# Performance work log

Measured on AMD Instinct MI355X. Metric: run time of the kernel, lower is better.

Reference implementation:

```python
import jax, jax.numpy as jnp
import numpy as np

B, N, C, H = 2, 8192, 256, 8  # Dh == C (attention_head_size = embedding_channels)
EPS = 1e-5  # InstanceNorm2d default eps


def setup_inputs() -> dict:
    key = jax.random.key(0)
    k1, k2, k3, k4, k5 = jax.random.split(key, 5)
    s = 1.0 / np.sqrt(C)
    return {
        "emb": jax.random.normal(k1, (B, N, C), dtype=jnp.float32),
        "Wq": jax.random.normal(k2, (C, C * H), dtype=jnp.float32) * s,
        "Wk": jax.random.normal(k3, (C, C * H), dtype=jnp.float32) * s,
        "Wv": jax.random.normal(k4, (C, C * H), dtype=jnp.float32) * s,
        "Wo": jax.random.normal(k5, (C * H, C), dtype=jnp.float32) * s,
    }


def reference(emb, Wq, Wk, Wv, Wo):
    b, n, c = emb.shape
    h = Wq.shape[1] // c  # num_heads; head_dim Dh == c

    def heads(x):  # [B,N,H*Dh] -> [B,H,N,Dh]
        return x.reshape(b, n, h, c).transpose(0, 2, 1, 3)

    qh = heads(emb @ Wq)  # [B,H,N,Dh]
    kh = heads(emb @ Wk)
    vh = heads(emb @ Wv)

    # channel attention: contract over sequence dim N -> [B,H,Dh,Dh]
    attn = jnp.einsum("bhnd,bhne->bhde", qh, kh)

    # InstanceNorm2d over the Dh x Dh map per (b,h), affine=False, biased var
    mu = attn.mean(axis=(2, 3), keepdims=True)
    var = attn.var(axis=(2, 3), keepdims=True)
    attn = (attn - mu) * jax.lax.rsqrt(var + EPS)

    attn = jax.nn.softmax(attn, axis=3)

    # attn @ v^T -> [B,H,Dh,N]
    ctx = jnp.einsum("bhde,bhne->bhdn", attn, vh)

    # permute(0,3,2,1) -> [B,N,Dh,H], flatten (Dh,H) -> KV_size
    ctx = ctx.transpose(0, 3, 2, 1).reshape(b, n, c * h)
    return ctx @ Wo  # [B,N,C]
```

## Files before the change

### kernel.cpp

```cpp
#include <hip/hip_runtime.h>
#include <hip/hip_bf16.h>

#define NB 2
#define NN 8192
#define NC 256
#define NH 8
#define NCH 2048

static constexpr float EPS = 1e-5f;


typedef __attribute__((ext_vector_type(8))) short bf16x8;
typedef __attribute__((ext_vector_type(4))) float f32x4;

#define MFMA16(a, b, c) __builtin_amdgcn_mfma_f32_16x16x32_bf16(a, b, c, 0, 0, 0)

static constexpr int ETH  = 0;
static constexpr int ETL  = 4194304;
static constexpr int WQTH = 8388608;
static constexpr int WQTL = 8912896;
static constexpr int WKTH = 9437184;
static constexpr int WKTL = 9961472;
static constexpr int WVH  = 10485760;
static constexpr int WVL  = 11010048;
static constexpr int WORH = 11534336;
static constexpr int WORL = 12058624;
static constexpr int GHH  = 12582912;
static constexpr int GHL  = 12713984;
static constexpr int T1H  = 12845056;
static constexpr int T1L  = 13893632;
static constexpr int SMH  = 14942208;
static constexpr int SML  = 15990784;
static constexpr int PTH  = 17039360;
static constexpr int PTL  = 17170432;


__device__ __forceinline__ ushort bf16rn(float x) {
    uint u = __float_as_uint(x);
    return (ushort)((u + 0x7fffu + ((u >> 16) & 1u)) >> 16);
}
__device__ __forceinline__ float bf2f(ushort h) { return __uint_as_float(((uint)h) << 16); }

__device__ __forceinline__ void stage64(ushort* __restrict__ lds, const ushort* __restrict__ src,
                                        int row0, int k0, int ld) {
    int t = threadIdx.x;
    int g = t & 7, r = t >> 3;
#pragma unroll
    for (int i = 0; i < 2; ++i, r += 32) {
        uint4 v = *(const uint4*)(src + (row0 + r) * ld + k0 + g * 8);
        *(uint4*)((char*)lds + r * 128 + ((g ^ (r & 7)) << 4)) = v;
    }
}

__device__ __forceinline__ void stage64_f32(ushort* __restrict__ ldsh, ushort* __restrict__ ldsl,
                                            const float* __restrict__ src, int row0, int k0, int ld) {
    int t = threadIdx.x;
    int g = t & 15, r = t >> 4;
#pragma unroll
    for (int i = 0; i < 4; ++i, r += 16) {
        float4 v = *(const float4*)(src + (row0 + r) * ld + k0 + g * 4);
        ushort h0 = bf16rn(v.x), h1 = bf16rn(v.y), h2 = bf16rn(v.z), h3 = bf16rn(v.w);
        ushort e0 = bf16rn(v.x - bf2f(h0)), e1 = bf16rn(v.y - bf2f(h1));
        ushort e2 = bf16rn(v.z - bf2f(h2)), e3 = bf16rn(v.w - bf2f(h3));
        int byte = r * 128 + ((((g >> 1) ^ (r & 7)) << 4) | ((g & 1) << 3));
        ushort4 hv = {h0, h1, h2, h3}, lv = {e0, e1, e2, e3};
        *(ushort4*)((char*)ldsh + byte) = hv;
        *(ushort4*)((char*)ldsl + byte) = lv;
    }
}

__device__ __forceinline__ bf16x8 frag64(const ushort* __restrict__ lds, int rbase, int ks) {
    int l = threadIdx.x & 63;
    int r = rbase + (l & 15);
    int slot = (ks * 4 + (l >> 4)) ^ (r & 7);
    return *(const bf16x8*)((const char*)lds + r * 128 + slot * 16);
}

__device__ __forceinline__ void mfma_tile(const ushort* Ah, const ushort* Al,
                                          const ushort* Bh, const ushort* Bl,
                                          int wm, int wn, f32x4 acc[2][2]) {
#pragma unroll
    for (int ks = 0; ks < 2; ++ks) {
        bf16x8 ah[2], al[2], bh[2], bl[2];
        ah[0] = frag64(Ah, wm, ks);      ah[1] = frag64(Ah, wm + 16, ks);
        al[0] = frag64(Al, wm, ks);      al[1] = frag64(Al, wm + 16, ks);
        bh[0] = frag64(Bh, wn, ks);      bh[1] = frag64(Bh, wn + 16, ks);
        bl[0] = frag64(Bl, wn, ks);      bl[1] = frag64(Bl, wn + 16, ks);
#pragma unroll
        for (int mi = 0; mi < 2; ++mi)
#pragma unroll
            for (int ni = 0; ni < 2; ++ni) {
                acc[mi][ni] = MFMA16(ah[mi], bh[ni], acc[mi][ni]);
                acc[mi][ni] = MFMA16(ah[mi], bl[ni], acc[mi][ni]);
                acc[mi][ni] = MFMA16(al[mi], bh[ni], acc[mi][ni]);
            }
    }
}

__device__ __forceinline__ void gemm_core(const ushort* Ahi, const ushort* Alo, int arow0, int lda, int k0a,
                                          const ushort* Bhi, const ushort* Blo, int brow0, int ldb, int k0b,
                                          int nkt, ushort* lds, f32x4 acc[2][2]) {
    ushort* Ah = lds; ushort* Al = lds + 4096; ushort* Bh = lds + 8192; ushort* Bl = lds + 12288;
    int w = threadIdx.x >> 6;
    int wm = (w >> 1) * 32, wn = (w & 1) * 32;
    for (int t = 0; t < nkt; ++t) {
        stage64(Ah, Ahi, arow0, k0a + t * 64, lda);
        stage64(Al, Alo, arow0, k0a + t * 64, lda);
        stage64(Bh, Bhi, brow0, k0b + t * 64, ldb);
        stage64(Bl, Blo, brow0, k0b + t * 64, ldb);
        __syncthreads();
        mfma_tile(Ah, Al, Bh, Bl, wm, wn, acc);
        __syncthreads();
    }
}

__device__ __forceinline__ void ep_hilo(ushort* Dh, ushort* Dl, int ld, int row0, int col0, f32x4 acc[2][2]) {
    int l = threadIdx.x & 63, w = threadIdx.x >> 6;
    int wm = (w >> 1) * 32, wn = (w & 1) * 32;
#pragma unroll
    for (int mi = 0; mi < 2; ++mi)
#pragma unroll
        for (int ni = 0; ni < 2; ++ni)
#pragma unroll
            for (int r = 0; r < 4; ++r) {
                float x = acc[mi][ni][r];
                int idx = (row0 + wm + mi * 16 + (l >> 4) * 4 + r) * ld + col0 + wn + ni * 16 + (l & 15);
                ushort h = bf16rn(x);
                Dh[idx] = h;
                Dl[idx] = bf16rn(x - bf2f(h));
            }
}

__device__ __forceinline__ void ep_f32(float* D, int ld, int row0, int col0, f32x4 acc[2][2]) {
    int l = threadIdx.x & 63, w = threadIdx.x >> 6;
    int wm = (w >> 1) * 32, wn = (w & 1) * 32;
#pragma unroll
    for (int mi = 0; mi < 2; ++mi)
#pragma unroll
        for (int ni = 0; ni < 2; ++ni)
#pragma unroll
            for (int r = 0; r < 4; ++r)
                D[(row0 + wm + mi * 16 + (l >> 4) * 4 + r) * ld + col0 + wn + ni * 16 + (l & 15)] = acc[mi][ni][r];
}


__global__ __launch_bounds__(256) void k_s0(const float* __restrict__ emb, ushort* __restrict__ us,
                                            float* __restrict__ stats) {
    __shared__ uint lds[64][65];
    int nt = blockIdx.x, ct = blockIdx.y, b = blockIdx.z;
    int t = threadIdx.x;
    if (nt == 0 && ct == 0 && b == 0 && t < 64) stats[t] = 0.f;
    const float* E = emb + b * (NN * NC);
    int n0 = nt * 64, c0 = ct * 64;
    int r = t >> 4, g = t & 15;
#pragma unroll
    for (int i = 0; i < 4; ++i) {
        int n = r + i * 16;
        float4 v = *(const float4*)(E + (n0 + n) * NC + c0 + g * 4);
        ushort h;
        h = bf16rn(v.x); lds[g * 4 + 0][n] = h | ((uint)bf16rn(v.x - bf2f(h)) << 16);
        h = bf16rn(v.y); lds[g * 4 + 1][n] = h | ((uint)bf16rn(v.y - bf2f(h)) << 16);
        h = bf16rn(v.z); lds[g * 4 + 2][n] = h | ((uint)bf16rn(v.z - bf2f(h)) << 16);
        h = bf16rn(v.w); lds[g * 4 + 3][n] = h | ((uint)bf16rn(v.w - bf2f(h)) << 16);
    }
    __syncthreads();
    ushort* EH = us + ETH + b * (NC * NN);
    ushort* EL = us + ETL + b * (NC * NN);
    int c = t >> 3, q = t & 7;
#pragma unroll
    for (int i = 0; i < 2; ++i) {
        int cc = c + i * 32;
        uint a0 = lds[cc][q * 8 + 0], a1 = lds[cc][q * 8 + 1], a2 = lds[cc][q * 8 + 2], a3 = lds[cc][q * 8 + 3];
        uint a4 = lds[cc][q * 8 + 4], a5 = lds[cc][q * 8 + 5], a6 = lds[cc][q * 8 + 6], a7 = lds[cc][q * 8 + 7];
        uint4 hv = {(a0 & 0xffffu) | (a1 << 16), (a2 & 0xffffu) | (a3 << 16),
                    (a4 & 0xffffu) | (a5 << 16), (a6 & 0xffffu) | (a7 << 16)};
        uint4 lv = {(a0 >> 16) | (a1 & 0xffff0000u), (a2 >> 16) | (a3 & 0xffff0000u),
                    (a4 >> 16) | (a5 & 0xffff0000u), (a6 >> 16) | (a7 & 0xffff0000u)};
        *(uint4*)(EH + (c0 + cc) * NN + n0 + q * 8) = hv;
        *(uint4*)(EL + (c0 + cc) * NN + n0 + q * 8) = lv;
    }
}

__global__ __launch_bounds__(256) void k_s1(const float* __restrict__ wq, const float* __restrict__ wk,
                                            ushort* __restrict__ us) {
    __shared__ uint lds[64][65];
    int jt = blockIdx.x, ct = blockIdx.y, z = blockIdx.z;
    const float* W = z ? wk : wq;
    ushort* DH = us + (z ? WKTH : WQTH);
    ushort* DL = us + (z ? WKTL : WQTL);
    int t = threadIdx.x, j0 = jt * 64, c0 = ct * 64;
    int r = t >> 4, g = t & 15;
#pragma unroll
    for (int i = 0; i < 4; ++i) {
        int c = r + i * 16;
        float4 v = *(const float4*)(W + (c0 + c) * NCH + j0 + g * 4);
        ushort h;
        h = bf16rn(v.x); lds[g * 4 + 0][c] = h | ((uint)bf16rn(v.x - bf2f(h)) << 16);
        h = bf16rn(v.y); lds[g * 4 + 1][c] = h | ((uint)bf16rn(v.y - bf2f(h)) << 16);
        h = bf16rn(v.z); lds[g * 4 + 2][c] = h | ((uint)bf16rn(v.z - bf2f(h)) << 16);
        h = bf16rn(v.w); lds[g * 4 + 3][c] = h | ((uint)bf16rn(v.w - bf2f(h)) << 16);
    }
    __syncthreads();
    int j = t >> 3, q = t & 7;
#pragma unroll
    for (int i = 0; i < 2; ++i) {
        int jj = j + i * 32;
        uint a0 = lds[jj][q * 8 + 0], a1 = lds[jj][q * 8 + 1], a2 = lds[jj][q * 8 + 2], a3 = lds[jj][q * 8 + 3];
        uint a4 = lds[jj][q * 8 + 4], a5 = lds[jj][q * 8 + 5], a6 = lds[jj][q * 8 + 6], a7 = lds[jj][q * 8 + 7];
        uint4 hv = {(a0 & 0xffffu) | (a1 << 16), (a2 & 0xffffu) | (a3 << 16),
                    (a4 & 0xffffu) | (a5 << 16), (a6 & 0xffffu) | (a7 << 16)};
        uint4 lv = {(a0 >> 16) | (a1 & 0xffff0000u), (a2 >> 16) | (a3 & 0xffff0000u),
                    (a4 >> 16) | (a5 & 0xffff0000u), (a6 >> 16) | (a7 & 0xffff0000u)};
        *(uint4*)(DH + (j0 + jj) * NC + c0 + q * 8) = hv;
        *(uint4*)(DL + (j0 + jj) * NC + c0 + q * 8) = lv;
    }
}

__global__ __launch_bounds__(256) void k_s1b(const float* __restrict__ wo, ushort* __restrict__ us) {
    __shared__ uint lds[64][65];
    int jt = blockIdx.x, dt = blockIdx.y, h = blockIdx.z;
    int t = threadIdx.x, j0 = jt * 64, d0 = dt * 64;
    int r = t >> 4, g = t & 15;
#pragma unroll
    for (int i = 0; i < 4; ++i) {
        int d = r + i * 16;
        float4 v = *(const float4*)(wo + ((d0 + d) * 8 + h) * NC + j0 + g * 4);
        ushort hh;
        hh = bf16rn(v.x); lds[g * 4 + 0][d] = hh | ((uint)bf16rn(v.x - bf2f(hh)) << 16);
        hh = bf16rn(v.y); lds[g * 4 + 1][d] = hh | ((uint)bf16rn(v.y - bf2f(hh)) << 16);
        hh = bf16rn(v.z); lds[g * 4 + 2][d] = hh | ((uint)bf16rn(v.z - bf2f(hh)) << 16);
        hh = bf16rn(v.w); lds[g * 4 + 3][d] = hh | ((uint)bf16rn(v.w - bf2f(hh)) << 16);
    }
    __syncthreads();
    int j = t >> 3, q = t & 7;
#pragma unroll
    for (int i = 0; i < 2; ++i) {
        int jj = j + i * 32;
        uint a0 = lds[jj][q * 8 + 0], a1 = lds[jj][q * 8 + 1], a2 = lds[jj][q * 8 + 2], a3 = lds[jj][q * 8 + 3];
        uint a4 = lds[jj][q * 8 + 4], a5 = lds[jj][q * 8 + 5], a6 = lds[jj][q * 8 + 6], a7 = lds[jj][q * 8 + 7];
        uint4 hv = {(a0 & 0xffffu) | (a1 << 16), (a2 & 0xffffu) | (a3 << 16),
                    (a4 & 0xffffu) | (a5 << 16), (a6 & 0xffffu) | (a7 << 16)};
        uint4 lv = {(a0 >> 16) | (a1 & 0xffff0000u), (a2 >> 16) | (a3 & 0xffff0000u),
                    (a4 >> 16) | (a5 & 0xffff0000u), (a6 >> 16) | (a7 & 0xffff0000u)};
        *(uint4*)(us + WORH + h * 65536 + (j0 + jj) * NC + d0 + q * 8) = hv;
        *(uint4*)(us + WORL + h * 65536 + (j0 + jj) * NC + d0 + q * 8) = lv;
    }
}

__global__ __launch_bounds__(256) void k_splitv(const float* __restrict__ wv, ushort* __restrict__ us) {
    int i = (blockIdx.x * 256 + threadIdx.x) * 4;
    float4 v = *(const float4*)(wv + i);
    ushort h0 = bf16rn(v.x), h1 = bf16rn(v.y), h2 = bf16rn(v.z), h3 = bf16rn(v.w);
    ushort e0 = bf16rn(v.x - bf2f(h0)), e1 = bf16rn(v.y - bf2f(h1));
    ushort e2 = bf16rn(v.z - bf2f(h2)), e3 = bf16rn(v.w - bf2f(h3));
    ushort4 hv = {h0, h1, h2, h3}, lv = {e0, e1, e2, e3};
    *(ushort4*)(us + WVH + i) = hv;
    *(ushort4*)(us + WVL + i) = lv;
}

__global__ __launch_bounds__(256) void k_gram(const ushort* __restrict__ us, float* __restrict__ gp) {
    __shared__ ushort lds[16384];
    int tile = blockIdx.x, kc = blockIdx.y, b = blockIdx.z;
    int c1 = (tile >> 2) * 64, c2 = (tile & 3) * 64;
    const ushort* eh = us + ETH + b * (NC * NN);
    const ushort* el = us + ETL + b * (NC * NN);
    f32x4 acc[2][2] = {{{0.f, 0.f, 0.f, 0.f}, {0.f, 0.f, 0.f, 0.f}},
                       {{0.f, 0.f, 0.f, 0.f}, {0.f, 0.f, 0.f, 0.f}}};
    gemm_core(eh, el, c1, NN, kc * 512, eh, el, c2, NN, kc * 512, 8, lds, acc);
    ep_f32(gp + (b * 16 + kc) * 65536, NC, c1, c2, acc);
}

__global__ __launch_bounds__(256) void k_s2(const float* __restrict__ gp, ushort* __restrict__ us) {
    int b = blockIdx.y;
    int i = (blockIdx.x * 256 + threadIdx.x) * 4;
    const float* src = gp + b * 16 * 65536 + i;
    float4 s = {0.f, 0.f, 0.f, 0.f};
#pragma unroll
    for (int kc = 0; kc < 16; ++kc) {
        float4 v = *(const float4*)(src + kc * 65536);
        s.x += v.x; s.y += v.y; s.z += v.z; s.w += v.w;
    }
    ushort h0 = bf16rn(s.x), h1 = bf16rn(s.y), h2 = bf16rn(s.z), h3 = bf16rn(s.w);
    ushort e0 = bf16rn(s.x - bf2f(h0)), e1 = bf16rn(s.y - bf2f(h1));
    ushort e2 = bf16rn(s.z - bf2f(h2)), e3 = bf16rn(s.w - bf2f(h3));
    ushort4 hv = {h0, h1, h2, h3}, lv = {e0, e1, e2, e3};
    *(ushort4*)(us + GHH + b * 65536 + i) = hv;
    *(ushort4*)(us + GHL + b * 65536 + i) = lv;
}

__global__ __launch_bounds__(256) void k_t1(ushort* __restrict__ us) {
    __shared__ ushort lds[16384];
    int mt = blockIdx.x, nt = blockIdx.y, b = blockIdx.z;
    f32x4 acc[2][2] = {{{0.f, 0.f, 0.f, 0.f}, {0.f, 0.f, 0.f, 0.f}},
                       {{0.f, 0.f, 0.f, 0.f}, {0.f, 0.f, 0.f, 0.f}}};
    gemm_core(us + WQTH, us + WQTL, mt * 64, NC, 0,
              us + GHH + b * 65536, us + GHL + b * 65536, nt * 64, NC, 0, 4, lds, acc);
    ep_hilo(us + T1H + b * 524288, us + T1L + b * 524288, NC, mt * 64, nt * 64, acc);
}

__global__ __launch_bounds__(256) void k_attn(ushort* __restrict__ us, float* __restrict__ attn,
                                              float* __restrict__ stats) {
    __shared__ ushort lds[16384];
    int tile = blockIdx.x, bh = blockIdx.y;
    int b = bh >> 3, h = bh & 7;
    int row0 = (tile >> 2) * 64, col0 = (tile & 3) * 64;
    f32x4 acc[2][2] = {{{0.f, 0.f, 0.f, 0.f}, {0.f, 0.f, 0.f, 0.f}},
                       {{0.f, 0.f, 0.f, 0.f}, {0.f, 0.f, 0.f, 0.f}}};
    gemm_core(us + T1H + b * 524288, us + T1L + b * 524288, h * 256 + row0, NC, 0,
              us + WKTH, us + WKTL, h * 256 + col0, NC, 0, 4, lds, acc);
    float* D = attn + bh * 65536;
    int l = threadIdx.x & 63, w = threadIdx.x >> 6;
    int wm = (w >> 1) * 32, wn = (w & 1) * 32;
    float lsum = 0.f, lss = 0.f;
#pragma unroll
    for (int mi = 0; mi < 2; ++mi)
#pragma unroll
        for (int ni = 0; ni < 2; ++ni)
#pragma unroll
            for (int r = 0; r < 4; ++r) {
                float x = acc[mi][ni][r];
                D[(row0 + wm + mi * 16 + (l >> 4) * 4 + r) * NC + col0 + wn + ni * 16 + (l & 15)] = x;
                lsum += x; lss += x * x;
            }
#pragma unroll
    for (int o = 32; o > 0; o >>= 1) { lsum += __shfl_xor(lsum, o); lss += __shfl_xor(lss, o); }
    if (l == 0) { atomicAdd(&stats[bh * 2], lsum); atomicAdd(&stats[bh * 2 + 1], lss); }
}

__global__ __launch_bounds__(256) void k_sm(const float* __restrict__ attn, const float* __restrict__ stats,
                                            ushort* __restrict__ us) {
    int bh = blockIdx.x, rb = blockIdx.y;
    float mean = stats[bh * 2] * (1.f / 65536.f);
    float var = stats[bh * 2 + 1] * (1.f / 65536.f) - mean * mean;
    float rs = rsqrtf(var + EPS);
    int w = threadIdx.x >> 6, l = threadIdx.x & 63;
    const float* src = attn + bh * 65536;
    ushort* dh = us + SMH + bh * 65536;
    ushort* dl = us + SML + bh * 65536;
    for (int rr = 0; rr < 16; ++rr) {
        int row = rb * 64 + w * 16 + rr;
        float4 v = *(const float4*)(src + row * 256 + l * 4);
        v.x *= rs; v.y *= rs; v.z *= rs; v.w *= rs;
        float mx = fmaxf(fmaxf(v.x, v.y), fmaxf(v.z, v.w));
#pragma unroll
        for (int o = 32; o > 0; o >>= 1) mx = fmaxf(mx, __shfl_xor(mx, o));
        float e0 = __expf(v.x - mx), e1 = __expf(v.y - mx), e2 = __expf(v.z - mx), e3 = __expf(v.w - mx);
        float se = e0 + e1 + e2 + e3;
#pragma unroll
        for (int o = 32; o > 0; o >>= 1) se += __shfl_xor(se, o);
        float inv = 1.f / se;
        e0 *= inv; e1 *= inv; e2 *= inv; e3 *= inv;
        ushort h0 = bf16rn(e0), h1 = bf16rn(e1), h2 = bf16rn(e2), h3 = bf16rn(e3);
        ushort f0 = bf16rn(e0 - bf2f(h0)), f1 = bf16rn(e1 - bf2f(h1));
        ushort f2 = bf16rn(e2 - bf2f(h2)), f3 = bf16rn(e3 - bf2f(h3));
        ushort4 hv = {h0, h1, h2, h3}, lv = {f0, f1, f2, f3};
        *(ushort4*)(dh + row * 256 + l * 4) = hv;
        *(ushort4*)(dl + row * 256 + l * 4) = lv;
    }
}

__global__ __launch_bounds__(256) void k_m(ushort* __restrict__ us) {
    __shared__ ushort lds[16384];
    int tile = blockIdx.x, bh = blockIdx.y;
    int h = bh & 7;
    int c0 = (tile >> 2) * 64, d0 = (tile & 3) * 64;
    f32x4 acc[2][2] = {{{0.f, 0.f, 0.f, 0.f}, {0.f, 0.f, 0.f, 0.f}},
                       {{0.f, 0.f, 0.f, 0.f}, {0.f, 0.f, 0.f, 0.f}}};
    gemm_core(us + WVH, us + WVL, c0, NCH, h * 256,
              us + SMH + bh * 65536, us + SML + bh * 65536, d0, NC, 0, 4, lds, acc);
    ep_hilo(us + T1H + bh * 65536, us + T1L + bh * 65536, NC, c0, d0, acc);
}

__global__ __launch_bounds__(256) void k_pt(ushort* __restrict__ us, float* __restrict__ ptp) {
    __shared__ ushort lds[16384];
    int tile = blockIdx.x, bh = blockIdx.y;
    int h = bh & 7;
    int j0 = (tile >> 2) * 64, c0 = (tile & 3) * 64;
    f32x4 acc[2][2] = {{{0.f, 0.f, 0.f, 0.f}, {0.f, 0.f, 0.f, 0.f}},
                       {{0.f, 0.f, 0.f, 0.f}, {0.f, 0.f, 0.f, 0.f}}};
    gemm_core(us + WORH + h * 65536, us + WORL + h * 65536, j0, NC, 0,
              us + T1H + bh * 65536, us + T1L + bh * 65536, c0, NC, 0, 4, lds, acc);
    ep_f32(ptp + bh * 65536, NC, j0, c0, acc);
}

__global__ __launch_bounds__(256) void k_s4(const float* __restrict__ ptp, ushort* __restrict__ us) {
    int b = blockIdx.y;
    int i = (blockIdx.x * 256 + threadIdx.x) * 4;
    const float* src = ptp + b * 8 * 65536 + i;
    float4 s = {0.f, 0.f, 0.f, 0.f};
#pragma unroll
    for (int h = 0; h < 8; ++h) {
        float4 v = *(const float4*)(src + h * 65536);
        s.x += v.x; s.y += v.y; s.z += v.z; s.w += v.w;
    }
    ushort h0 = bf16rn(s.x), h1 = bf16rn(s.y), h2 = bf16rn(s.z), h3 = bf16rn(s.w);
    ushort e0 = bf16rn(s.x - bf2f(h0)), e1 = bf16rn(s.y - bf2f(h1));
    ushort e2 = bf16rn(s.z - bf2f(h2)), e3 = bf16rn(s.w - bf2f(h3));
    ushort4 hv = {h0, h1, h2, h3}, lv = {e0, e1, e2, e3};
    *(ushort4*)(us + PTH + b * 65536 + i) = hv;
    *(ushort4*)(us + PTL + b * 65536 + i) = lv;
}

__global__ __launch_bounds__(256) void k_out(const float* __restrict__ emb, const ushort* __restrict__ us,
                                             float* __restrict__ out) {
    __shared__ ushort lds[16384];
    ushort* Ah = lds; ushort* Al = lds + 4096; ushort* Bh = lds + 8192; ushort* Bl = lds + 12288;
    int nt = blockIdx.x, jt = blockIdx.y, b = blockIdx.z;
    const float* E = emb + b * (NN * NC);
    const ushort* PH = us + PTH + b * 65536;
    const ushort* PL = us + PTL + b * 65536;
    int w = threadIdx.x >> 6;
    int wm = (w >> 1) * 32, wn = (w & 1) * 32;
    f32x4 acc[2][2] = {{{0.f, 0.f, 0.f, 0.f}, {0.f, 0.f, 0.f, 0.f}},
                       {{0.f, 0.f, 0.f, 0.f}, {0.f, 0.f, 0.f, 0.f}}};
    for (int t = 0; t < 4; ++t) {
        stage64_f32(Ah, Al, E, nt * 64, t * 64, NC);
        stage64(Bh, PH, jt * 64, t * 64, NC);
        stage64(Bl, PL, jt * 64, t * 64, NC);
        __syncthreads();
        mfma_tile(Ah, Al, Bh, Bl, wm, wn, acc);
        __syncthreads();
    }
    ep_f32(out + b * (NN * NC), NC, nt * 64, jt * 64, acc);
}


extern "C" void kernel_launch(void* const* d_in, const int* in_sizes, int n_in,
                              void* d_out, int out_size, void* d_ws, size_t ws_size,
                              hipStream_t stream) {
    const float* emb = (const float*)d_in[0];
    const float* Wq  = (const float*)d_in[1];
    const float* Wk  = (const float*)d_in[2];
    const float* Wv  = (const float*)d_in[3];
    const float* Wo  = (const float*)d_in[4];
    float* out = (float*)d_out;
    float* ws  = (float*)d_ws;

    float* Gp    = ws;
    float* attn  = ws;
    float* Ptp   = ws + 1048576;
    float* stats = ws + 2097152;
    ushort* us   = (ushort*)(ws + 2097216);

    k_s0    <<<dim3(128, 4, NB), dim3(256), 0, stream>>>(emb, us, stats);
    k_s1    <<<dim3(32, 4, 2),   dim3(256), 0, stream>>>(Wq, Wk, us);
    k_s1b   <<<dim3(4, 4, 8),    dim3(256), 0, stream>>>(Wo, us);
    k_splitv<<<dim3(512),        dim3(256), 0, stream>>>(Wv, us);
    k_gram  <<<dim3(16, 16, NB), dim3(256), 0, stream>>>(us, Gp);
    k_s2    <<<dim3(64, NB),     dim3(256), 0, stream>>>(Gp, us);
    k_t1    <<<dim3(32, 4, NB),  dim3(256), 0, stream>>>(us);
    k_attn  <<<dim3(16, 16),     dim3(256), 0, stream>>>(us, attn, stats);
    k_sm    <<<dim3(16, 4),      dim3(256), 0, stream>>>(attn, stats, us);
    k_m     <<<dim3(16, 16),     dim3(256), 0, stream>>>(us);
    k_pt    <<<dim3(16, 16),     dim3(256), 0, stream>>>(us, Ptp);
    k_s4    <<<dim3(64, NB),     dim3(256), 0, stream>>>(Ptp, us);
    k_out   <<<dim3(128, 4, NB), dim3(256), 0, stream>>>(emb, us, out);
}
```

Before: 176.3 us.

## Fuse emb split into Gram kernel, exploit symmetry, merge weight prep kernels

Measured after the change: 216.1 us. +22.6%, slower.

```diff
diff --git a/kernel.cpp b/kernel.cpp
--- a/kernel.cpp
+++ b/kernel.cpp
@@ -15,24 +15,22 @@
 
 #define MFMA16(a, b, c) __builtin_amdgcn_mfma_f32_16x16x32_bf16(a, b, c, 0, 0, 0)
 
-static constexpr int ETH  = 0;
-static constexpr int ETL  = 4194304;
-static constexpr int WQTH = 8388608;
-static constexpr int WQTL = 8912896;
-static constexpr int WKTH = 9437184;
-static constexpr int WKTL = 9961472;
-static constexpr int WVH  = 10485760;
-static constexpr int WVL  = 11010048;
-static constexpr int WORH = 11534336;
-static constexpr int WORL = 12058624;
-static constexpr int GHH  = 12582912;
-static constexpr int GHL  = 12713984;
-static constexpr int T1H  = 12845056;
-static constexpr int T1L  = 13893632;
-static constexpr int SMH  = 14942208;
-static constexpr int SML  = 15990784;
-static constexpr int PTH  = 17039360;
-static constexpr int PTL  = 17170432;
+static constexpr int WQTH = 0;
+static constexpr int WQTL = 524288;
+static constexpr int WKTH = 1048576;
+static constexpr int WKTL = 1572864;
+static constexpr int WVH  = 2097152;
+static constexpr int WVL  = 2621440;
+static constexpr int WORH = 3145728;
+static constexpr int WORL = 3670016;
+static constexpr int GHH  = 4194304;
+static constexpr int GHL  = 4325376;
+static constexpr int T1H  = 4456448;
+static constexpr int T1L  = 5505024;
+static constexpr int SMH  = 6553600;
+static constexpr int SML  = 7602176;
+static constexpr int PTH  = 8650752;
+static constexpr int PTL  = 8781824;
 
 
 __device__ __forceinline__ ushort bf16rn(float x) {
@@ -69,6 +67,29 @@
     }
 }
 
+__device__ __forceinline__ void stage_tr(ushort* __restrict__ ldsh, ushort* __restrict__ ldsl,
+                                         const float* __restrict__ E, int n0, int cb) {
+    int l = threadIdx.x & 63, w = threadIdx.x >> 6;
+    const float* src = E + (n0 + w * 16) * NC + cb + l;
+    float v[16];
+#pragma unroll
+    for (int j = 0; j < 16; ++j) v[j] = src[j * NC];
+    int rowbyte = l * 128;
+#pragma unroll
+    for (int qq = 0; qq < 4; ++qq) {
+        int q = (qq + (l >> 3)) & 3;
+        int n = w * 16 + q * 4;
+        float a0 = v[q * 4], a1 = v[q * 4 + 1], a2 = v[q * 4 + 2], a3 = v[q * 4 + 3];
+        ushort h0 = bf16rn(a0), h1 = bf16rn(a1), h2 = bf16rn(a2), h3 = bf16rn(a3);
+        ushort e0 = bf16rn(a0 - bf2f(h0)), e1 = bf16rn(a1 - bf2f(h1));
+        ushort e2 = bf16rn(a2 - bf2f(h2)), e3 = bf16rn(a3 - bf2f(h3));
+        int byte = rowbyte + ((((n >> 3) ^ (l & 7)) << 4) | ((n & 4) << 1));
+        ushort4 hv = {h0, h1, h2, h3}, lv = {e0, e1, e2, e3};
+        *(ushort4*)((char*)ldsh + byte) = hv;
+        *(ushort4*)((char*)ldsl + byte) = lv;
+    }
+}
+
 __device__ __forceinline__ bf16x8 frag64(const ushort* __restrict__ lds, int rbase, int ks) {
     int l = threadIdx.x & 63;
     int r = rbase + (l & 15);
@@ -143,62 +164,19 @@
                 D[(row0 + wm + mi * 16 + (l >> 4) * 4 + r) * ld + col0 + wn + ni * 16 + (l & 15)] = acc[mi][ni][r];
 }
 
-
-__global__ __launch_bounds__(256) void k_s0(const float* __restrict__ emb, ushort* __restrict__ us,
-                                            float* __restrict__ stats) {
-    __shared__ uint lds[64][65];
-    int nt = blockIdx.x, ct = blockIdx.y, b = blockIdx.z;
+__device__ __forceinline__ void tsplit(uint (*lds)[65], const float* __restrict__ src, int srcStride,
+                                       ushort* __restrict__ DH, ushort* __restrict__ DL) {
     int t = threadIdx.x;
-    if (nt == 0 && ct == 0 && b == 0 && t < 64) stats[t] = 0.f;
-    const float* E = emb + b * (NN * NC);
-    int n0 = nt * 64, c0 = ct * 64;
     int r = t >> 4, g = t & 15;
 #pragma unroll
     for (int i = 0; i < 4; ++i) {
-        int n = r + i * 16;
-        float4 v = *(const float4*)(E + (n0 + n) * NC + c0 + g * 4);
+        int m = r + i * 16;
+        float4 v = *(const float4*)(src + m * srcStride + g * 4);
         ushort h;
-        h = bf16rn(v.x); lds[g * 4 + 0][n] = h | ((uint)bf16rn(v.x - bf2f(h)) << 16);
-        h = bf16rn(v.y); lds[g * 4 + 1][n] = h | ((uint)bf16rn(v.y - bf2f(h)) << 16);
-        h = bf16rn(v.z); lds[g * 4 + 2][n] = h | ((uint)bf16rn(v.z - bf2f(h)) << 16);
-        h = bf16rn(v.w); lds[g * 4 + 3][n] = h | ((uint)bf16rn(v.w - bf2f(h)) << 16);
-    }
-    __syncthreads();
-    ushort* EH = us + ETH + b * (NC * NN);
-    ushort* EL = us + ETL + b * (NC * NN);
-    int c = t >> 3, q = t & 7;
-#pragma unroll
-    for (int i = 0; i < 2; ++i) {
-        int cc = c + i * 32;
-        uint a0 = lds[cc][q * 8 + 0], a1 = lds[cc][q * 8 + 1], a2 = lds[cc][q * 8 + 2], a3 = lds[cc][q * 8 + 3];
-        uint a4 = lds[cc][q * 8 + 4], a5 = lds[cc][q * 8 + 5], a6 = lds[cc][q * 8 + 6], a7 = lds[cc][q * 8 + 7];
-        uint4 hv = {(a0 & 0xffffu) | (a1 << 16), (a2 & 0xffffu) | (a3 << 16),
-                    (a4 & 0xffffu) | (a5 << 16), (a6 & 0xffffu) | (a7 << 16)};
-        uint4 lv = {(a0 >> 16) | (a1 & 0xffff0000u), (a2 >> 16) | (a3 & 0xffff0000u),
-                    (a4 >> 16) | (a5 & 0xffff0000u), (a6 >> 16) | (a7 & 0xffff0000u)};
-        *(uint4*)(EH + (c0 + cc) * NN + n0 + q * 8) = hv;
-        *(uint4*)(EL + (c0 + cc) * NN + n0 + q * 8) = lv;
-    }
-}
-
-__global__ __launch_bounds__(256) void k_s1(const float* __restrict__ wq, const float* __restrict__ wk,
-                                            ushort* __restrict__ us) {
-    __shared__ uint lds[64][65];
-    int jt = blockIdx.x, ct = blockIdx.y, z = blockIdx.z;
-    const float* W = z ? wk : wq;
-    ushort* DH = us + (z ? WKTH : WQTH);
-    ushort* DL = us + (z ? WKTL : WQTL);
-    int t = threadIdx.x, j0 = jt * 64, c0 = ct * 64;
-    int r = t >> 4, g = t & 15;
-#pragma unroll
-    for (int i = 0; i < 4; ++i) {
-        int c = r + i * 16;
-        float4 v = *(const float4*)(W + (c0 + c) * NCH + j0 + g * 4);
-        ushort h;
-        h = bf16rn(v.x); lds[g * 4 + 0][c] = h | ((uint)bf16rn(v.x - bf2f(h)) << 16);
-        h = bf16rn(v.y); lds[g * 4 + 1][c] = h | ((uint)bf16rn(v.y - bf2f(h)) << 16);
-        h = bf16rn(v.z); lds[g * 4 + 2][c] = h | ((uint)bf16rn(v.z - bf2f(h)) << 16);
-        h = bf16rn(v.w); lds[g * 4 + 3][c] = h | ((uint)bf16rn(v.w - bf2f(h)) << 16);
+        h = bf16rn(v.x); lds[g * 4 + 0][m] = h | ((uint)bf16rn(v.x - bf2f(h)) << 16);
+        h = bf16rn(v.y); lds[g * 4 + 1][m] = h | ((uint)bf16rn(v.y - bf2f(h)) << 16);
+        h = bf16rn(v.z); lds[g * 4 + 2][m] = h | ((uint)bf16rn(v.z - bf2f(h)) << 16);
+        h = bf16rn(v.w); lds[g * 4 + 3][m] = h | ((uint)bf16rn(v.w - bf2f(h)) << 16);
     }
     __syncthreads();
     int j = t >> 3, q = t & 7;
@@ -211,81 +189,114 @@
                     (a4 & 0xffffu) | (a5 << 16), (a6 & 0xffffu) | (a7 << 16)};
         uint4 lv = {(a0 >> 16) | (a1 & 0xffff0000u), (a2 >> 16) | (a3 & 0xffff0000u),
                     (a4 >> 16) | (a5 & 0xffff0000u), (a6 >> 16) | (a7 & 0xffff0000u)};
-        *(uint4*)(DH + (j0 + jj) * NC + c0 + q * 8) = hv;
-        *(uint4*)(DL + (j0 + jj) * NC + c0 + q * 8) = lv;
-    }
-}
-
-__global__ __launch_bounds__(256) void k_s1b(const float* __restrict__ wo, ushort* __restrict__ us) {
+        *(uint4*)(DH + jj * NC + q * 8) = hv;
+        *(uint4*)(DL + jj * NC + q * 8) = lv;
+    }
+}
+
+
+__global__ __launch_bounds__(256) void k_prep(const float* __restrict__ wq, const float* __restrict__ wk,
+                                              const float* __restrict__ wv, const float* __restrict__ wo,
+                                              ushort* __restrict__ us, float* __restrict__ stats) {
     __shared__ uint lds[64][65];
-    int jt = blockIdx.x, dt = blockIdx.y, h = blockIdx.z;
-    int t = threadIdx.x, j0 = jt * 64, d0 = dt * 64;
-    int r = t >> 4, g = t & 15;
-#pragma unroll
-    for (int i = 0; i < 4; ++i) {
-        int d = r + i * 16;
-        float4 v = *(const float4*)(wo + ((d0 + d) * 8 + h) * NC + j0 + g * 4);
-        ushort hh;
-        hh = bf16rn(v.x); lds[g * 4 + 0][d] = hh | ((uint)bf16rn(v.x - bf2f(hh)) << 16);
-        hh = bf16rn(v.y); lds[g * 4 + 1][d] = hh | ((uint)bf16rn(v.y - bf2f(hh)) << 16);
-        hh = bf16rn(v.z); lds[g * 4 + 2][d] = hh | ((uint)bf16rn(v.z - bf2f(hh)) << 16);
-        hh = bf16rn(v.w); lds[g * 4 + 3][d] = hh | ((uint)bf16rn(v.w - bf2f(hh)) << 16);
-    }
-    __syncthreads();
-    int j = t >> 3, q = t & 7;
-#pragma unroll
-    for (int i = 0; i < 2; ++i) {
-        int jj = j + i * 32;
-        uint a0 = lds[jj][q * 8 + 0], a1 = lds[jj][q * 8 + 1], a2 = lds[jj][q * 8 + 2], a3 = lds[jj][q * 8 + 3];
-        uint a4 = lds[jj][q * 8 + 4], a5 = lds[jj][q * 8 + 5], a6 = lds[jj][q * 8 + 6], a7 = lds[jj][q * 8 + 7];
-        uint4 hv = {(a0 & 0xffffu) | (a1 << 16), (a2 & 0xffffu) | (a3 << 16),
-                    (a4 & 0xffffu) | (a5 << 16), (a6 & 0xffffu) | (a7 << 16)};
-        uint4 lv = {(a0 >> 16) | (a1 & 0xffff0000u), (a2 >> 16) | (a3 & 0xffff0000u),
-                    (a4 >> 16) | (a5 & 0xffff0000u), (a6 >> 16) | (a7 & 0xffff0000u)};
-        *(uint4*)(us + WORH + h * 65536 + (j0 + jj) * NC + d0 + q * 8) = hv;
-        *(uint4*)(us + WORL + h * 65536 + (j0 + jj) * NC + d0 + q * 8) = lv;
-    }
-}
-
-__global__ __launch_bounds__(256) void k_splitv(const float* __restrict__ wv, ushort* __restrict__ us) {
-    int i = (blockIdx.x * 256 + threadIdx.x) * 4;
-    float4 v = *(const float4*)(wv + i);
-    ushort h0 = bf16rn(v.x), h1 = bf16rn(v.y), h2 = bf16rn(v.z), h3 = bf16rn(v.w);
-    ushort e0 = bf16rn(v.x - bf2f(h0)), e1 = bf16rn(v.y - bf2f(h1));
-    ushort e2 = bf16rn(v.z - bf2f(h2)), e3 = bf16rn(v.w - bf2f(h3));
-    ushort4 hv = {h0, h1, h2, h3}, lv = {e0, e1, e2, e3};
-    *(ushort4*)(us + WVH + i) = hv;
-    *(ushort4*)(us + WVL + i) = lv;
-}
-
-__global__ __launch_bounds__(256) void k_gram(const ushort* __restrict__ us, float* __restrict__ gp) {
+    int x = blockIdx.x, z = blockIdx.y;
+    int t = threadIdx.x;
+    if (z == 3) {
+        if (x == 0 && t < 64) stats[t] = 0.f;
+        int i = (x * 256 + t) * 4;
+        float4 v = *(const float4*)(wv + i);
+        ushort h0 = bf16rn(v.x), h1 = bf16rn(v.y), h2 = bf16rn(v.z), h3 = bf16rn(v.w);
+        ushort e0 = bf16rn(v.x - bf2f(h0)), e1 = bf16rn(v.y - bf2f(h1));
+        ushort e2 = bf16rn(v.z - bf2f(h2)), e3 = bf16rn(v.w - bf2f(h3));
+        ushort4 hv = {h0, h1, h2, h3}, lv = {e0, e1, e2, e3};
+        *(ushort4*)(us + WVH + i) = hv;
+        *(ushort4*)(us + WVL + i) = lv;
+        return;
+    }
+    if (x >= 128) return;
+    if (z == 2) {
+        int h = x >> 4, dt = (x >> 2) & 3, jt = x & 3;
+        tsplit(lds, wo + (dt * 64 * 8 + h) * NC + jt * 64, 8 * NC,
+               us + WORH + h * 65536 + (jt * 64) * NC + dt * 64,
+               us + WORL + h * 65536 + (jt * 64) * NC + dt * 64);
+        return;
+    }
+    int jt = x >> 2, ct = x & 3;
+    const float* W = z ? wk : wq;
+    int dh = (z ? WKTH : WQTH) + (jt * 64) * NC + ct * 64;
+    int dl = (z ? WKTL : WQTL) + (jt * 64) * NC + ct * 64;
+    tsplit(lds, W + (ct * 64) * NCH + jt * 64, NCH, us + dh, us + dl);
+}
+
+static __device__ const int TI1[10] = {0, 0, 0, 0, 1, 1, 1, 2, 2, 3};
+static __device__ const int TI2[10] = {0, 1, 2, 3, 1, 2, 3, 2, 3, 3};
+
+__global__ __launch_bounds__(256) void k_gram(const float* __restrict__ emb, float* __restrict__ gp) {
     __shared__ ushort lds[16384];
     int tile = blockIdx.x, kc = blockIdx.y, b = blockIdx.z;
-    int c1 = (tile >> 2) * 64, c2 = (tile & 3) * 64;
-    const ushort* eh = us + ETH + b * (NC * NN);
-    const ushort* el = us + ETL + b * (NC * NN);
-    f32x4 acc[2][2] = {{{0.f, 0.f, 0.f, 0.f}, {0.f, 0.f, 0.f, 0.f}},
-                       {{0.f, 0.f, 0.f, 0.f}, {0.f, 0.f, 0.f, 0.f}}};
-    gemm_core(eh, el, c1, NN, kc * 512, eh, el, c2, NN, kc * 512, 8, lds, acc);
-    ep_f32(gp + (b * 16 + kc) * 65536, NC, c1, c2, acc);
+    int c1 = TI1[tile] * 64, c2 = TI2[tile] * 64;
+    bool diag = (c1 == c2);
+    const float* E = emb + b * (NN * NC);
+    ushort* Ah = lds; ushort* Al = lds + 4096; ushort* Bh = lds + 8192; ushort* Bl = lds + 12288;
+    int w = threadIdx.x >> 6;
+    int wm = (w >> 1) * 32, wn = (w & 1) * 32;
+    f32x4 acc[2][2] = {{{0.f, 0.f, 0.f, 0.f}, {0.f, 0.f, 0.f, 0.f}},
+                       {{0.f, 0.f, 0.f, 0.f}, {0.f, 0.f, 0.f, 0.f}}};
+    for (int kb = 0; kb < 8; ++kb) {
+        int n0 = kc * 512 + kb * 64;
+        stage_tr(Ah, Al, E, n0, c1);
+        if (!diag) stage_tr(Bh, Bl, E, n0, c2);
+        __syncthreads();
+        mfma_tile(Ah, Al, diag ? Ah : Bh, diag ? Al : Bl, wm, wn, acc);
+        __syncthreads();
+    }
+    ep_f32(gp + ((b * 16 + kc) * 10 + tile) * 4096, 64, 0, 0, acc);
 }
 
 __global__ __launch_bounds__(256) void k_s2(const float* __restrict__ gp, ushort* __restrict__ us) {
-    int b = blockIdx.y;
-    int i = (blockIdx.x * 256 + threadIdx.x) * 4;
-    const float* src = gp + b * 16 * 65536 + i;
-    float4 s = {0.f, 0.f, 0.f, 0.f};
-#pragma unroll
+    __shared__ float T[64][65];
+    int tile = blockIdx.x, b = blockIdx.y;
+    int c1 = TI1[tile] * 64, c2 = TI2[tile] * 64;
+    int t = threadIdx.x;
+    const float* src = gp + (b * 160 + tile) * 4096;
+    ushort* GH = us + GHH + b * 65536;
+    ushort* GL = us + GHL + b * 65536;
+    float4 s[4] = {{0.f, 0.f, 0.f, 0.f}, {0.f, 0.f, 0.f, 0.f}, {0.f, 0.f, 0.f, 0.f}, {0.f, 0.f, 0.f, 0.f}};
     for (int kc = 0; kc < 16; ++kc) {
-        float4 v = *(const float4*)(src + kc * 65536);
-        s.x += v.x; s.y += v.y; s.z += v.z; s.w += v.w;
-    }
-    ushort h0 = bf16rn(s.x), h1 = bf16rn(s.y), h2 = bf16rn(s.z), h3 = bf16rn(s.w);
-    ushort e0 = bf16rn(s.x - bf2f(h0)), e1 = bf16rn(s.y - bf2f(h1));
-    ushort e2 = bf16rn(s.z - bf2f(h2)), e3 = bf16rn(s.w - bf2f(h3));
-    ushort4 hv = {h0, h1, h2, h3}, lv = {e0, e1, e2, e3};
-    *(ushort4*)(us + GHH + b * 65536 + i) = hv;
-    *(ushort4*)(us + GHL + b * 65536 + i) = lv;
+        const float4* p = (const float4*)(src + kc * 40960);
+#pragma unroll
+        for (int k2 = 0; k2 < 4; ++k2) {
+            float4 v = p[t + k2 * 256];
+            s[k2].x += v.x; s[k2].y += v.y; s[k2].z += v.z; s[k2].w += v.w;
+        }
+    }
+#pragma unroll
+    for (int k2 = 0; k2 < 4; ++k2) {
+        int f = t + k2 * 256;
+        int r = f >> 4, c = (f & 15) * 4;
+        ushort h0 = bf16rn(s[k2].x), h1 = bf16rn(s[k2].y), h2 = bf16rn(s[k2].z), h3 = bf16rn(s[k2].w);
+        ushort e0 = bf16rn(s[k2].x - bf2f(h0)), e1 = bf16rn(s[k2].y - bf2f(h1));
+        ushort e2 = bf16rn(s[k2].z - bf2f(h2)), e3 = bf16rn(s[k2].w - bf2f(h3));
+        ushort4 hv = {h0, h1, h2, h3}, lv = {e0, e1, e2, e3};
+        *(ushort4*)(GH + (c1 + r) * NC + c2 + c) = hv;
+        *(ushort4*)(GL + (c1 + r) * NC + c2 + c) = lv;
+        T[r][c + 0] = s[k2].x; T[r][c + 1] = s[k2].y; T[r][c + 2] = s[k2].z; T[r][c + 3] = s[k2].w;
+    }
+    if (c1 != c2) {
+        __syncthreads();
+#pragma unroll
+        for (int k2 = 0; k2 < 4; ++k2) {
+            int f = t + k2 * 256;
+            int r = f >> 4, c = (f & 15) * 4;
+            float a0 = T[c + 0][r], a1 = T[c + 1][r], a2 = T[c + 2][r], a3 = T[c + 3][r];
+            ushort h0 = bf16rn(a0), h1 = bf16rn(a1), h2 = bf16rn(a2), h3 = bf16rn(a3);
+            ushort e0 = bf16rn(a0 - bf2f(h0)), e1 = bf16rn(a1 - bf2f(h1));
+            ushort e2 = bf16rn(a2 - bf2f(h2)), e3 = bf16rn(a3 - bf2f(h3));
+            ushort4 hv = {h0, h1, h2, h3}, lv = {e0, e1, e2, e3};
+            *(ushort4*)(GH + (c2 + r) * NC + c1 + c) = hv;
+            *(ushort4*)(GL + (c2 + r) * NC + c1 + c) = lv;
+        }
+    }
 }
 
 __global__ __launch_bounds__(256) void k_t1(ushort* __restrict__ us) {
@@ -438,21 +449,18 @@
 
     float* Gp    = ws;
     float* attn  = ws;
-    float* Ptp   = ws + 1048576;
-    float* stats = ws + 2097152;
-    ushort* us   = (ushort*)(ws + 2097216);
-
-    k_s0    <<<dim3(128, 4, NB), dim3(256), 0, stream>>>(emb, us, stats);
-    k_s1    <<<dim3(32, 4, 2),   dim3(256), 0, stream>>>(Wq, Wk, us);
-    k_s1b   <<<dim3(4, 4, 8),    dim3(256), 0, stream>>>(Wo, us);
-    k_splitv<<<dim3(512),        dim3(256), 0, stream>>>(Wv, us);
-    k_gram  <<<dim3(16, 16, NB), dim3(256), 0, stream>>>(us, Gp);
-    k_s2    <<<dim3(64, NB),     dim3(256), 0, stream>>>(Gp, us);
-    k_t1    <<<dim3(32, 4, NB),  dim3(256), 0, stream>>>(us);
-    k_attn  <<<dim3(16, 16),     dim3(256), 0, stream>>>(us, attn, stats);
-    k_sm    <<<dim3(16, 4),      dim3(256), 0, stream>>>(attn, stats, us);
-    k_m     <<<dim3(16, 16),     dim3(256), 0, stream>>>(us);
-    k_pt    <<<dim3(16, 16),     dim3(256), 0, stream>>>(us, Ptp);
-    k_s4    <<<dim3(64, NB),     dim3(256), 0, stream>>>(Ptp, us);
-    k_out   <<<dim3(128, 4, NB), dim3(256), 0, stream>>>(emb, us, out);
-}
+    float* Ptp   = ws + 1310720;
+    float* stats = ws + 2359296;
+    ushort* us   = (ushort*)(ws + 2359360);
+
+    k_prep<<<dim3(512, 4),    dim3(256), 0, stream>>>(Wq, Wk, Wv, Wo, us, stats);
+    k_gram<<<dim3(10, 16, NB), dim3(256), 0, stream>>>(emb, Gp);
+    k_s2  <<<dim3(10, NB),     dim3(256), 0, stream>>>(Gp, us);
+    k_t1  <<<dim3(32, 4, NB),  dim3(256), 0, stream>>>(us);
+    k_attn<<<dim3(16, 16),     dim3(256), 0, stream>>>(us, attn, stats);
+    k_sm  <<<dim3(16, 4),      dim3(256), 0, stream>>>(attn, stats, us);
+    k_m   <<<dim3(16, 16),     dim3(256), 0, stream>>>(us);
+    k_pt  <<<dim3(16, 16),     dim3(256), 0, stream>>>(us, Ptp);
+    k_s4  <<<dim3(64, NB),     dim3(256), 0, stream>>>(Ptp, us);
+    k_out <<<dim3(128, 4, NB), dim3(256), 0, stream>>>(emb, us, out);
+}
```
